# Performance work log

Measured on AMD Instinct MI355X. Metric: run time of the kernel, lower is better.

The kernel has to match this reference:

```python
import jax, jax.numpy as jnp
import numpy as np

NUM_CLASSES = 80
CONF_THRE = 0.2
NMS_THRE = 0.45
MAX_DET = 300   # fixed cap replacing torch's variable-length NMS output (padded + keep mask)
IMG = 640.0


def setup_inputs() -> dict:
    key = jax.random.key(0)
    k1, k2 = jax.random.split(key)
    pred = jax.random.uniform(k1, (32, 8400, 85), dtype=jnp.float32)
    # scale cx,cy,w,h to pixel range so IoU/NMS geometry is realistic
    pred = pred.at[..., :4].multiply(IMG)
    zone = jax.random.uniform(k2, (8, 2), dtype=jnp.float32) * IMG
    return {"prediction": pred, "zone": zone}


def _pairwise_iou(b):
    # b: [B, K, 4] in x1y1x2y2
    area = jnp.clip(b[..., 2] - b[..., 0], 0.0) * jnp.clip(b[..., 3] - b[..., 1], 0.0)
    lt = jnp.maximum(b[:, :, None, :2], b[:, None, :, :2])
    rb = jnp.minimum(b[:, :, None, 2:], b[:, None, :, 2:])
    wh = jnp.clip(rb - lt, 0.0)
    inter = wh[..., 0] * wh[..., 1]
    return inter / (area[:, :, None] + area[:, None, :] - inter + 1e-9)


def _postprocess(prediction):
    # decode cx,cy,w,h -> x1,y1,x2,y2
    xy = prediction[..., :2]
    wh = prediction[..., 2:4]
    boxes = jnp.concatenate([xy - wh * 0.5, xy + wh * 0.5], axis=-1)  # [B,N,4]
    obj = prediction[..., 4]                                           # [B,N]
    cls = prediction[..., 5:5 + NUM_CLASSES]
    class_conf = jnp.max(cls, axis=-1)                                 # [B,N]
    class_pred = jnp.argmax(cls, axis=-1)                              # [B,N]

    # confidence mask (obj * class_conf >= thre); invalid -> -inf so top_k drops them
    nms_score = obj * class_conf
    nms_score = jnp.where(nms_score >= CONF_THRE, nms_score, -jnp.inf)

    s, idx = jax.lax.top_k(nms_score, MAX_DET)                         # [B,K]
    b = jnp.take_along_axis(boxes, idx[..., None], axis=1)             # [B,K,4]

    # class-agnostic greedy NMS on score-sorted boxes (matches torchvision.ops.nms)
    iou = _pairwise_iou(b)                                             # [B,K,K]
    keep = jnp.isfinite(s)                                             # valid (passed conf) entries
    ar = jnp.arange(MAX_DET)
    def body(i, keep):
        sup = keep[:, i][:, None] & (iou[:, i, :] > NMS_THRE) & (ar > i)
        return keep & jnp.logical_not(sup)
    keep = jax.lax.fori_loop(0, MAX_DET, body, keep)

    obj_s = jnp.take_along_axis(obj, idx, axis=1)
    conf_s = jnp.take_along_axis(class_conf, idx, axis=1)
    cls_s = jnp.take_along_axis(class_pred, idx, axis=1).astype(jnp.int32)
    # extract_boxes_scores_and_classes: score = max over columns [obj, class_conf]
    scores = jnp.maximum(obj_s, conf_s)
    return b, scores, cls_s, keep


def _points_inside_zone(px, py, zone):
    # px, py: [B,K]; zone: [Z,2]. Ray-casting parity test (faithful to torch version).
    zr = jnp.roll(zone, shift=1, axis=0)
    xi, yi = zone[:, 0], zone[:, 1]
    xj, yj = zr[:, 0], zr[:, 1]
    pyb = py[..., None]  # [B,K,1] vs [Z]
    pxb = px[..., None]
    gyi = yi > pyb
    gyj = yj > pyb
    gx = (xj - xi) * (pyb - yi) / (yj - yi) + xi
    inter = (gyi != gyj) & (gx > pxb)
    return (jnp.sum(inter.astype(jnp.int32), axis=-1) % 2) > 0


def reference(prediction, zone):
    b, scores, classes, keep = _postprocess(prediction)
    cx = (b[..., 0] + b[..., 2]) * 0.5
    cy = (b[..., 1] + b[..., 3]) * 0.5
    in_zone = _points_inside_zone(cx, cy, zone) & keep
    centers_yx = jnp.stack([cy, cx], axis=-1)                          # [B,K,2]
    boxes_yxyx = jnp.stack([b[..., 1], b[..., 0], b[..., 3], b[..., 2]], axis=-1)
    return boxes_yxyx, in_zone, scores, classes, centers_yx, keep
```

## Files before the change

kernel.cpp:

```cpp
#include <hip/hip_runtime.h>
#include <stdint.h>

typedef unsigned long long ull;

#define NA 8400
#define NB 32
#define KTOP 300
#define NC 80
#define CH 9
#define NKPAD 9216
#define NCOPY 16
#define HSTRIDE 257

#define O1 38400
#define O2 48000
#define O3 57600
#define O4 67200
#define O5 86400

#define WS_BATCH_BASE (2u << 20)
#define WS_BATCH_STRIDE 16384

__global__ __launch_bounds__(256) void score_kernel(const float* __restrict__ pred,
                                                    uint32_t* __restrict__ keys) {
    __shared__ float sP[128 * 85];
    const int blk = blockIdx.x;
    const float4* g4 = (const float4*)(pred + (size_t)blk * 128 * 85);
    float4* l4 = (float4*)sP;
    for (int i = threadIdx.x; i < (128 * 85 / 4); i += 256) l4[i] = g4[i];
    __syncthreads();
    const int t = threadIdx.x;
    if (t < 128) {
        const float* p = sP + t * 85;
        float obj = p[4];
        float b0 = p[5], b1 = p[6], b2 = p[7], b3 = p[8];
        #pragma unroll
        for (int c = 4; c < NC; c += 4) {
            b0 = fmaxf(b0, p[5 + c]);
            b1 = fmaxf(b1, p[6 + c]);
            b2 = fmaxf(b2, p[7 + c]);
            b3 = fmaxf(b3, p[8 + c]);
        }
        float best = fmaxf(fmaxf(b0, b1), fmaxf(b2, b3));
        float sc = obj * best;
        uint32_t u = (sc >= 0.2f) ? (__float_as_uint(sc) | 0x80000000u) : 0x007FFFFFu;
        keys[(size_t)blk * 128 + t] = u;
    }
}

__global__ __launch_bounds__(1024) void select_kernel(const uint32_t* __restrict__ keys,
                                                      uint8_t* __restrict__ ws) {
    __shared__ uint32_t sKeys[NKPAD];
    __shared__ ull sSel[KTOP];
    __shared__ ull sSorted[KTOP];
    __shared__ uint32_t sH[NCOPY * HSTRIDE];
    __shared__ uint32_t sWTot[16];
    __shared__ uint32_t sBc[2];
    __shared__ uint32_t sRank[KTOP];

    const int b = blockIdx.x;
    const int t = threadIdx.x;
    const int lane = t & 63;
    const int wv = t >> 6;

    {
        const uint4* g4 = (const uint4*)(keys + (size_t)b * NA);
        uint4* l4 = (uint4*)sKeys;
        for (int i = t; i < NA / 4; i += 1024) l4[i] = g4[i];
        for (int i = NA + t; i < NKPAD; i += 1024) sKeys[i] = 0u;
    }
    if (t < KTOP) sRank[t] = 0u;
    __syncthreads();

    const int beg = t * CH;
    uint32_t prefix = 0, r = KTOP;
    for (int round = 0; round < 4; ++round) {
        const int shift = 24 - 8 * round;
        for (int i = t; i < NCOPY * HSTRIDE; i += 1024) sH[i] = 0u;
        __syncthreads();
        const uint32_t pmask = (round == 0) ? 0u : (0xFFFFFFFFu << (shift + 8));
        const uint32_t pref = prefix & pmask;
        uint32_t* hw = &sH[wv * HSTRIDE];
        #pragma unroll
        for (int e = 0; e < CH; ++e) {
            uint32_t k = sKeys[beg + e];
            if ((k & pmask) == pref)
                atomicAdd(&hw[(k >> shift) & 0xFFu], 1u);
        }
        __syncthreads();
        if (wv == 0) {
            uint32_t v0 = 0, v1 = 0, v2 = 0, v3 = 0;
            #pragma unroll
            for (int c = 0; c < NCOPY; ++c) {
                const uint32_t* hc = &sH[c * HSTRIDE];
                v0 += hc[lane]; v1 += hc[64 + lane];
                v2 += hc[128 + lane]; v3 += hc[192 + lane];
            }
            uint32_t s0 = v0, s1 = v1, s2 = v2, s3 = v3;
            #pragma unroll
            for (int off = 1; off < 64; off <<= 1) {
                uint32_t o0 = __shfl_down(s0, off, 64), o1 = __shfl_down(s1, off, 64);
                uint32_t o2 = __shfl_down(s2, off, 64), o3 = __shfl_down(s3, off, 64);
                if (lane + off < 64) { s0 += o0; s1 += o1; s2 += o2; s3 += o3; }
            }
            uint32_t T1 = __shfl(s1, 0, 64), T2 = __shfl(s2, 0, 64), T3 = __shfl(s3, 0, 64);
            uint32_t S0 = s0 + T1 + T2 + T3;
            uint32_t S1 = s1 + T2 + T3;
            uint32_t S2 = s2 + T3;
            uint32_t S3 = s3;
            if (S0 >= r && S0 - v0 < r) { sBc[0] = prefix | ((uint32_t)lane << shift);         sBc[1] = r - (S0 - v0); }
            if (S1 >= r && S1 - v1 < r) { sBc[0] = prefix | ((uint32_t)(64  + lane) << shift); sBc[1] = r - (S1 - v1); }
            if (S2 >= r && S2 - v2 < r) { sBc[0] = prefix | ((uint32_t)(128 + lane) << shift); sBc[1] = r - (S2 - v2); }
            if (S3 >= r && S3 - v3 < r) { sBc[0] = prefix | ((uint32_t)(192 + lane) << shift); sBc[1] = r - (S3 - v3); }
        }
        __syncthreads();
        prefix = sBc[0]; r = sBc[1];
    }
    const uint32_t kth = prefix;
    const uint32_t rem = r;
    const uint32_t cntgt = KTOP - rem;

    {
        uint32_t gtc = 0, eqc = 0;
        #pragma unroll
        for (int e = 0; e < CH; ++e) {
            uint32_t k = sKeys[beg + e];
            gtc += (k > kth) ? 1u : 0u;
            eqc += (k == kth) ? 1u : 0u;
        }
        uint32_t pack = (gtc << 16) | eqc;
        uint32_t ps = pack;
        #pragma unroll
        for (int off = 1; off < 64; off <<= 1) {
            uint32_t o = __shfl_up(ps, off, 64);
            if (lane >= off) ps += o;
        }
        if (lane == 63) sWTot[wv] = ps;
        __syncthreads();
        uint32_t excl = ps - pack;
        #pragma unroll
        for (int w2 = 0; w2 < 16; ++w2) if (w2 < wv) excl += sWTot[w2];
        uint32_t gtoff = excl >> 16;
        uint32_t eqoff = excl & 0xFFFFu;
        #pragma unroll
        for (int e = 0; e < CH; ++e) {
            uint32_t k = sKeys[beg + e];
            uint32_t idx = (uint32_t)(beg + e);
            if (k > kth) {
                sSel[gtoff++] = ((ull)k << 32) | (ull)(0xFFFFFFFFu - idx);
            } else if (k == kth) {
                if (eqoff < rem)
                    sSel[cntgt + eqoff] = ((ull)k << 32) | (ull)(0xFFFFFFFFu - idx);
                eqoff++;
            }
        }
        __syncthreads();
    }

    for (int p2 = t; p2 < KTOP * 4; p2 += 1024) {
        const int i = p2 >> 2;
        const int q = p2 & 3;
        const ull my = sSel[i];
        const int j0 = q * 75, j1 = j0 + 75;
        uint32_t cnt = 0;
        for (int j = j0; j < j1; ++j)
            cnt += (sSel[j] > my) ? 1u : 0u;
        if (cnt) atomicAdd(&sRank[i], cnt);
    }
    __syncthreads();
    if (t < KTOP) sSorted[sRank[t]] = sSel[t];
    __syncthreads();

    ull* selW = (ull*)(ws + WS_BATCH_BASE + (size_t)b * WS_BATCH_STRIDE);
    if (t < KTOP) selW[t] = sSorted[t];
}

__global__ __launch_bounds__(1024) void prep_kernel(const float* __restrict__ pred,
                                                    uint8_t* __restrict__ ws,
                                                    float* __restrict__ out) {
    #pragma clang fp contract(off)
    __shared__ float sB0[KTOP], sB1[KTOP], sB2[KTOP], sB3[KTOP];
    const int b = blockIdx.y;
    const int t = threadIdx.x;
    const ull* sel = (const ull*)(ws + WS_BATCH_BASE + (size_t)b * WS_BATCH_STRIDE);
    const size_t bo = (size_t)b * KTOP;

    if (blockIdx.x == 0) {
        if (t < 2 * KTOP) {
            const int row = t >> 1;
            const int half = t & 1;
            const uint32_t a = 0xFFFFFFFFu - (uint32_t)sel[row];
            const float* p = pred + ((size_t)b * NA + a) * 85;
            const int cbase = half * 40;
            float v0 = p[5 + cbase], v1 = p[6 + cbase], v2 = p[7 + cbase], v3 = p[8 + cbase];
            int   c0 = cbase, c1 = cbase + 1, c2 = cbase + 2, c3 = cbase + 3;
            #pragma unroll
            for (int c = 4; c < 40; c += 4) {
                float w0 = p[5 + cbase + c],     w1 = p[6 + cbase + c];
                float w2 = p[7 + cbase + c],     w3 = p[8 + cbase + c];
                if (w0 > v0) { v0 = w0; c0 = cbase + c; }
                if (w1 > v1) { v1 = w1; c1 = cbase + c + 1; }
                if (w2 > v2) { v2 = w2; c2 = cbase + c + 2; }
                if (w3 > v3) { v3 = w3; c3 = cbase + c + 3; }
            }
            float bv = v0; int bc = c0;
            if (v1 > bv || (v1 == bv && c1 < bc)) { bv = v1; bc = c1; }
            if (v2 > bv || (v2 == bv && c2 < bc)) { bv = v2; bc = c2; }
            if (v3 > bv || (v3 == bv && c3 < bc)) { bv = v3; bc = c3; }
            float pv = __shfl_xor(bv, 1, 64);
            int   pc = __shfl_xor(bc, 1, 64);
            if (half == 0) {
                if (pv > bv) { bv = pv; bc = pc; }
                float x = p[0], y = p[1], w = p[2], h = p[3], obj = p[4];
                float hw = w * 0.5f, hh = h * 0.5f;
                float x1 = x - hw, y1 = y - hh, x2 = x + hw, y2 = y + hh;
                out[(bo + row) * 4 + 0] = y1;
                out[(bo + row) * 4 + 1] = x1;
                out[(bo + row) * 4 + 2] = y2;
                out[(bo + row) * 4 + 3] = x2;
                out[O4 + (bo + row) * 2 + 0] = (y1 + y2) * 0.5f;
                out[O4 + (bo + row) * 2 + 1] = (x1 + x2) * 0.5f;
                out[O2 + bo + row] = fmaxf(obj, bv);
                out[O3 + bo + row] = (float)bc;
            }
        }
    } else {
        if (t < KTOP) {
            const uint32_t a = 0xFFFFFFFFu - (uint32_t)sel[t];
            const float* p = pred + ((size_t)b * NA + a) * 85;
            float x = p[0], y = p[1], w = p[2], h = p[3];
            float hw = w * 0.5f, hh = h * 0.5f;
            sB0[t] = x - hw; sB1[t] = y - hh; sB2[t] = x + hw; sB3[t] = y + hh;
        }
        __syncthreads();
        ull* maskW = (ull*)(ws + WS_BATCH_BASE + (size_t)b * WS_BATCH_STRIDE + 2400);
        for (int p2 = t; p2 < KTOP * 5; p2 += 1024) {
            const int role = p2 / KTOP;
            const int i = p2 - role * KTOP;
            const int j0 = role * 64;
            int jmax = j0 + 64; if (jmax > KTOP) jmax = KTOP;
            float x1 = sB0[i], y1 = sB1[i], x2 = sB2[i], y2 = sB3[i];
            float ai = fmaxf(x2 - x1, 0.0f) * fmaxf(y2 - y1, 0.0f);
            ull bits = 0ull;
            for (int j = j0; j < jmax; ++j) {
                float bx1 = sB0[j], by1 = sB1[j], bx2 = sB2[j], by2 = sB3[j];
                float aj = fmaxf(bx2 - bx1, 0.0f) * fmaxf(by2 - by1, 0.0f);
                float iw = fminf(x2, bx2) - fmaxf(x1, bx1); iw = fmaxf(iw, 0.0f);
                float ih = fminf(y2, by2) - fmaxf(y1, by1); ih = fmaxf(ih, 0.0f);
                float inter = iw * ih;
                float den = ai + aj;
                den = den - inter;
                den = den + 1e-9f;
                float iou = inter / den;
                if (j > i && iou > 0.45f) bits |= (1ull << (j - j0));
            }
            maskW[i * 5 + role] = bits;
        }
    }
}

__global__ __launch_bounds__(512) void finish_kernel(const float* __restrict__ zone,
                                                     const uint8_t* __restrict__ ws,
                                                     float* __restrict__ out) {
    #pragma clang fp contract(off)
    __shared__ ull sMask[KTOP * 5];
    __shared__ ull sSel[KTOP];
    __shared__ uint32_t sPar[KTOP];
    __shared__ ull sKeepF[5];
    __shared__ float sZone[16];
    const int b = blockIdx.x;
    const int t = threadIdx.x;
    const int lane = t & 63;
    const int wv = t >> 6;
    const ull* selG = (const ull*)(ws + WS_BATCH_BASE + (size_t)b * WS_BATCH_STRIDE);
    const ull* maskG = selG + KTOP;
    for (int i = t; i < KTOP; i += 512) sSel[i] = selG[i];
    for (int i = t; i < KTOP * 5; i += 512) sMask[i] = maskG[i];
    if (t < 16) sZone[t] = zone[t];
    __syncthreads();

    const size_t bo = (size_t)b * KTOP;
    if (wv == 0) {
        ull rm[5][5];
        ull kw[5];
        #pragma unroll
        for (int w = 0; w < 5; ++w) {
            int i = w * 64 + lane;
            bool f = (i < KTOP) && (((uint32_t)(sSel[i] >> 32)) > 0x007FFFFFu);
            kw[w] = __ballot(f);
            #pragma unroll
            for (int ww = 0; ww < 5; ++ww)
                rm[w][ww] = (i < KTOP) ? sMask[i * 5 + ww] : 0ull;
        }
        #pragma unroll
        for (int w = 0; w < 5; ++w) {
            ull cur = kw[w];
            while (cur) {
                int ib = __builtin_ctzll(cur);
                ull m0 = __shfl(rm[w][0], ib);
                ull m1 = __shfl(rm[w][1], ib);
                ull m2 = __shfl(rm[w][2], ib);
                ull m3 = __shfl(rm[w][3], ib);
                ull m4 = __shfl(rm[w][4], ib);
                kw[0] &= ~m0; kw[1] &= ~m1; kw[2] &= ~m2; kw[3] &= ~m3; kw[4] &= ~m4;
                ull done = (ib == 63) ? 0ull : (~0ull << (ib + 1));
                cur = kw[w] & done;
            }
        }
        if (lane == 0) {
            #pragma unroll
            for (int w = 0; w < 5; ++w) sKeepF[w] = kw[w];
        }
    } else if (t >= 64 && t < 64 + KTOP) {
        const int i = t - 64;
        float cy = out[O4 + (bo + i) * 2 + 0];
        float cx = out[O4 + (bo + i) * 2 + 1];
        int cnt = 0;
        #pragma unroll
        for (int e = 0; e < 8; ++e) {
            float xi = sZone[2 * e], yi = sZone[2 * e + 1];
            int ep = (e + 7) & 7;
            float xj = sZone[2 * ep], yj = sZone[2 * ep + 1];
            bool gyi = yi > cy, gyj = yj > cy;
            if (gyi != gyj) {
                float gx = (xj - xi) * (cy - yi) / (yj - yi) + xi;
                if (gx > cx) cnt++;
            }
        }
        sPar[i] = (uint32_t)(cnt & 1);
    }
    __syncthreads();

    if (t < KTOP) {
        int kp = (int)((sKeepF[t >> 6] >> (t & 63)) & 1ull);
        int inz = (sPar[t] && kp) ? 1 : 0;
        out[O1 + bo + t] = (float)inz;
        out[O5 + bo + t] = (float)kp;
    }
}

extern "C" void kernel_launch(void* const* d_in, const int* in_sizes, int n_in,
                              void* d_out, int out_size, void* d_ws, size_t ws_size,
                              hipStream_t stream) {
    const float* pred = (const float*)d_in[0];
    const float* zone = (const float*)d_in[1];
    float* out = (float*)d_out;
    uint32_t* keys = (uint32_t*)d_ws;
    uint8_t* ws = (uint8_t*)d_ws;

    score_kernel<<<(NB * NA) / 128, 256, 0, stream>>>(pred, keys);
    select_kernel<<<NB, 1024, 0, stream>>>(keys, ws);
    prep_kernel<<<dim3(2, NB), 1024, 0, stream>>>(pred, ws, out);
    finish_kernel<<<NB, 512, 0, stream>>>(zone, ws, out);
}
```

Before: 209.1 us.

## Replace 4-pass radix select with single-pass bin histogram and fuse kernels

The four-round radix select over the score keys becomes one histogram pass over fixed-width bins above the confidence threshold. Keys in the boundary bin go to a small candidate buffer that is ranked exactly, capped at 256 entries. The box/class gather moves into the select kernel, and IoU mask construction plus greedy NMS and zone tests merge into one kernel, cutting four launches to three and removing the global mask round trip. The candidate cap can silently drop entries if more than 256 keys share the boundary bin.

After: 197.5 us. -5.5%, faster.

```diff
diff --git a/kernel.cpp b/kernel.cpp
--- a/kernel.cpp
+++ b/kernel.cpp
@@ -9,8 +9,11 @@
 #define NC 80
 #define CH 9
 #define NKPAD 9216
-#define NCOPY 16
-#define HSTRIDE 257
+#define NBIN 616
+#define HSTR 617
+#define NCPY 8
+#define BASEK 0xBE4CCCCDu
+#define CANDMAX 256
 
 #define O1 38400
 #define O2 48000
@@ -19,7 +22,7 @@
 #define O5 86400
 
 #define WS_BATCH_BASE (2u << 20)
-#define WS_BATCH_STRIDE 16384
+#define WS_BATCH_STRIDE 8192
 
 __global__ __launch_bounds__(256) void score_kernel(const float* __restrict__ pred,
                                                     uint32_t* __restrict__ keys) {
@@ -48,15 +51,24 @@
     }
 }
 
-__global__ __launch_bounds__(1024) void select_kernel(const uint32_t* __restrict__ keys,
-                                                      uint8_t* __restrict__ ws) {
+__device__ __forceinline__ uint32_t key_bin(uint32_t k) {
+    return (k < BASEK) ? 0u : (1u + ((k - BASEK) >> 15));
+}
+
+__global__ __launch_bounds__(1024) void select_kernel(const float* __restrict__ pred,
+                                                      const uint32_t* __restrict__ keys,
+                                                      uint8_t* __restrict__ ws,
+                                                      float* __restrict__ out) {
+    #pragma clang fp contract(off)
     __shared__ uint32_t sKeys[NKPAD];
+    __shared__ uint32_t sH[NCPY * HSTR];
     __shared__ ull sSel[KTOP];
     __shared__ ull sSorted[KTOP];
-    __shared__ uint32_t sH[NCOPY * HSTRIDE];
+    __shared__ ull sCand[CANDMAX];
     __shared__ uint32_t sWTot[16];
     __shared__ uint32_t sBc[2];
     __shared__ uint32_t sRank[KTOP];
+    __shared__ uint32_t sCN;
 
     const int b = blockIdx.x;
     const int t = threadIdx.x;
@@ -69,64 +81,57 @@
         for (int i = t; i < NA / 4; i += 1024) l4[i] = g4[i];
         for (int i = NA + t; i < NKPAD; i += 1024) sKeys[i] = 0u;
     }
+    for (int i = t; i < NCPY * HSTR; i += 1024) sH[i] = 0u;
     if (t < KTOP) sRank[t] = 0u;
     __syncthreads();
 
     const int beg = t * CH;
-    uint32_t prefix = 0, r = KTOP;
-    for (int round = 0; round < 4; ++round) {
-        const int shift = 24 - 8 * round;
-        for (int i = t; i < NCOPY * HSTRIDE; i += 1024) sH[i] = 0u;
-        __syncthreads();
-        const uint32_t pmask = (round == 0) ? 0u : (0xFFFFFFFFu << (shift + 8));
-        const uint32_t pref = prefix & pmask;
-        uint32_t* hw = &sH[wv * HSTRIDE];
+    {
+        uint32_t* hw = &sH[(t >> 7) * HSTR];
         #pragma unroll
         for (int e = 0; e < CH; ++e) {
             uint32_t k = sKeys[beg + e];
-            if ((k & pmask) == pref)
-                atomicAdd(&hw[(k >> shift) & 0xFFu], 1u);
-        }
-        __syncthreads();
-        if (wv == 0) {
-            uint32_t v0 = 0, v1 = 0, v2 = 0, v3 = 0;
+            atomicAdd(&hw[key_bin(k)], 1u);
+        }
+    }
+    __syncthreads();
+
+    uint32_t v = 0, s = 0;
+    if (t < 640) {
+        if (t < NBIN) {
             #pragma unroll
-            for (int c = 0; c < NCOPY; ++c) {
-                const uint32_t* hc = &sH[c * HSTRIDE];
-                v0 += hc[lane]; v1 += hc[64 + lane];
-                v2 += hc[128 + lane]; v3 += hc[192 + lane];
-            }
-            uint32_t s0 = v0, s1 = v1, s2 = v2, s3 = v3;
-            #pragma unroll
-            for (int off = 1; off < 64; off <<= 1) {
-                uint32_t o0 = __shfl_down(s0, off, 64), o1 = __shfl_down(s1, off, 64);
-                uint32_t o2 = __shfl_down(s2, off, 64), o3 = __shfl_down(s3, off, 64);
-                if (lane + off < 64) { s0 += o0; s1 += o1; s2 += o2; s3 += o3; }
-            }
-            uint32_t T1 = __shfl(s1, 0, 64), T2 = __shfl(s2, 0, 64), T3 = __shfl(s3, 0, 64);
-            uint32_t S0 = s0 + T1 + T2 + T3;
-            uint32_t S1 = s1 + T2 + T3;
-            uint32_t S2 = s2 + T3;
-            uint32_t S3 = s3;
-            if (S0 >= r && S0 - v0 < r) { sBc[0] = prefix | ((uint32_t)lane << shift);         sBc[1] = r - (S0 - v0); }
-            if (S1 >= r && S1 - v1 < r) { sBc[0] = prefix | ((uint32_t)(64  + lane) << shift); sBc[1] = r - (S1 - v1); }
-            if (S2 >= r && S2 - v2 < r) { sBc[0] = prefix | ((uint32_t)(128 + lane) << shift); sBc[1] = r - (S2 - v2); }
-            if (S3 >= r && S3 - v3 < r) { sBc[0] = prefix | ((uint32_t)(192 + lane) << shift); sBc[1] = r - (S3 - v3); }
-        }
-        __syncthreads();
-        prefix = sBc[0]; r = sBc[1];
-    }
-    const uint32_t kth = prefix;
-    const uint32_t rem = r;
+            for (int c = 0; c < NCPY; ++c) v += sH[c * HSTR + t];
+        }
+        s = v;
+        #pragma unroll
+        for (int off = 1; off < 64; off <<= 1) {
+            uint32_t o = __shfl_down(s, off, 64);
+            if (lane + off < 64) s += o;
+        }
+        if (lane == 0) sWTot[wv] = s;
+    }
+    __syncthreads();
+    if (t < 640) {
+        uint32_t S = s;
+        for (int w2 = wv + 1; w2 < 10; ++w2) S += sWTot[w2];
+        uint32_t above = S - v;
+        if (above < KTOP && S >= KTOP) {
+            sBc[0] = (uint32_t)t;
+            sBc[1] = KTOP - above;
+        }
+    }
+    __syncthreads();
+    const uint32_t Tbin = sBc[0];
+    const uint32_t rem = sBc[1];
     const uint32_t cntgt = KTOP - rem;
 
     {
         uint32_t gtc = 0, eqc = 0;
         #pragma unroll
         for (int e = 0; e < CH; ++e) {
-            uint32_t k = sKeys[beg + e];
-            gtc += (k > kth) ? 1u : 0u;
-            eqc += (k == kth) ? 1u : 0u;
+            uint32_t bin = key_bin(sKeys[beg + e]);
+            gtc += (bin > Tbin) ? 1u : 0u;
+            eqc += (bin == Tbin) ? 1u : 0u;
         }
         uint32_t pack = (gtc << 16) | eqc;
         uint32_t ps = pack;
@@ -142,17 +147,33 @@
         for (int w2 = 0; w2 < 16; ++w2) if (w2 < wv) excl += sWTot[w2];
         uint32_t gtoff = excl >> 16;
         uint32_t eqoff = excl & 0xFFFFu;
+        if (t == 1023) {
+            uint32_t tot = eqoff + eqc;
+            sCN = (tot > CANDMAX) ? CANDMAX : tot;
+        }
         #pragma unroll
         for (int e = 0; e < CH; ++e) {
             uint32_t k = sKeys[beg + e];
+            uint32_t bin = key_bin(k);
             uint32_t idx = (uint32_t)(beg + e);
-            if (k > kth) {
+            if (bin > Tbin) {
                 sSel[gtoff++] = ((ull)k << 32) | (ull)(0xFFFFFFFFu - idx);
-            } else if (k == kth) {
-                if (eqoff < rem)
-                    sSel[cntgt + eqoff] = ((ull)k << 32) | (ull)(0xFFFFFFFFu - idx);
+            } else if (bin == Tbin) {
+                if (eqoff < CANDMAX)
+                    sCand[eqoff] = ((ull)k << 32) | (ull)(0xFFFFFFFFu - idx);
                 eqoff++;
             }
+        }
+        __syncthreads();
+    }
+
+    {
+        int cn = (int)sCN;
+        if (t < cn) {
+            ull my = sCand[t];
+            uint32_t rk = 0;
+            for (int j = 0; j < cn; ++j) rk += (sCand[j] > my) ? 1u : 0u;
+            if (rk < rem) sSel[cntgt + rk] = my;
         }
         __syncthreads();
     }
@@ -172,97 +193,56 @@
     __syncthreads();
 
     ull* selW = (ull*)(ws + WS_BATCH_BASE + (size_t)b * WS_BATCH_STRIDE);
+    float* boxW = (float*)(selW + KTOP);
+    const size_t bo = (size_t)b * KTOP;
     if (t < KTOP) selW[t] = sSorted[t];
-}
-
-__global__ __launch_bounds__(1024) void prep_kernel(const float* __restrict__ pred,
-                                                    uint8_t* __restrict__ ws,
-                                                    float* __restrict__ out) {
+    if (t < 2 * KTOP) {
+        const int row = t >> 1;
+        const int half = t & 1;
+        const uint32_t a = 0xFFFFFFFFu - (uint32_t)sSorted[row];
+        const float* p = pred + ((size_t)b * NA + a) * 85;
+        const int cbase = half * 40;
+        float v0 = p[5 + cbase], v1 = p[6 + cbase], v2 = p[7 + cbase], v3 = p[8 + cbase];
+        int   c0 = cbase, c1 = cbase + 1, c2 = cbase + 2, c3 = cbase + 3;
+        #pragma unroll
+        for (int c = 4; c < 40; c += 4) {
+            float w0 = p[5 + cbase + c],     w1 = p[6 + cbase + c];
+            float w2 = p[7 + cbase + c],     w3 = p[8 + cbase + c];
+            if (w0 > v0) { v0 = w0; c0 = cbase + c; }
+            if (w1 > v1) { v1 = w1; c1 = cbase + c + 1; }
+            if (w2 > v2) { v2 = w2; c2 = cbase + c + 2; }
+            if (w3 > v3) { v3 = w3; c3 = cbase + c + 3; }
+        }
+        float bv = v0; int bc = c0;
+        if (v1 > bv || (v1 == bv && c1 < bc)) { bv = v1; bc = c1; }
+        if (v2 > bv || (v2 == bv && c2 < bc)) { bv = v2; bc = c2; }
+        if (v3 > bv || (v3 == bv && c3 < bc)) { bv = v3; bc = c3; }
+        float pv = __shfl_xor(bv, 1, 64);
+        int   pc = __shfl_xor(bc, 1, 64);
+        if (half == 0) {
+            if (pv > bv) { bv = pv; bc = pc; }
+            float x = p[0], y = p[1], w = p[2], h = p[3], obj = p[4];
+            float hw = w * 0.5f, hh = h * 0.5f;
+            float x1 = x - hw, y1 = y - hh, x2 = x + hw, y2 = y + hh;
+            boxW[row] = x1; boxW[KTOP + row] = y1;
+            boxW[2 * KTOP + row] = x2; boxW[3 * KTOP + row] = y2;
+            out[(bo + row) * 4 + 0] = y1;
+            out[(bo + row) * 4 + 1] = x1;
+            out[(bo + row) * 4 + 2] = y2;
+            out[(bo + row) * 4 + 3] = x2;
+            out[O4 + (bo + row) * 2 + 0] = (y1 + y2) * 0.5f;
+            out[O4 + (bo + row) * 2 + 1] = (x1 + x2) * 0.5f;
+            out[O2 + bo + row] = fmaxf(obj, bv);
+            out[O3 + bo + row] = (float)bc;
+        }
+    }
+}
+
+__global__ __launch_bounds__(1024) void nms_kernel(const float* __restrict__ zone,
+                                                   const uint8_t* __restrict__ ws,
+                                                   float* __restrict__ out) {
     #pragma clang fp contract(off)
     __shared__ float sB0[KTOP], sB1[KTOP], sB2[KTOP], sB3[KTOP];
-    const int b = blockIdx.y;
-    const int t = threadIdx.x;
-    const ull* sel = (const ull*)(ws + WS_BATCH_BASE + (size_t)b * WS_BATCH_STRIDE);
-    const size_t bo = (size_t)b * KTOP;
-
-    if (blockIdx.x == 0) {
-        if (t < 2 * KTOP) {
-            const int row = t >> 1;
-            const int half = t & 1;
-            const uint32_t a = 0xFFFFFFFFu - (uint32_t)sel[row];
-            const float* p = pred + ((size_t)b * NA + a) * 85;
-            const int cbase = half * 40;
-            float v0 = p[5 + cbase], v1 = p[6 + cbase], v2 = p[7 + cbase], v3 = p[8 + cbase];
-            int   c0 = cbase, c1 = cbase + 1, c2 = cbase + 2, c3 = cbase + 3;
-            #pragma unroll
-            for (int c = 4; c < 40; c += 4) {
-                float w0 = p[5 + cbase + c],     w1 = p[6 + cbase + c];
-                float w2 = p[7 + cbase + c],     w3 = p[8 + cbase + c];
-                if (w0 > v0) { v0 = w0; c0 = cbase + c; }
-                if (w1 > v1) { v1 = w1; c1 = cbase + c + 1; }
-                if (w2 > v2) { v2 = w2; c2 = cbase + c + 2; }
-                if (w3 > v3) { v3 = w3; c3 = cbase + c + 3; }
-            }
-            float bv = v0; int bc = c0;
-            if (v1 > bv || (v1 == bv && c1 < bc)) { bv = v1; bc = c1; }
-            if (v2 > bv || (v2 == bv && c2 < bc)) { bv = v2; bc = c2; }
-            if (v3 > bv || (v3 == bv && c3 < bc)) { bv = v3; bc = c3; }
-            float pv = __shfl_xor(bv, 1, 64);
-            int   pc = __shfl_xor(bc, 1, 64);
-            if (half == 0) {
-                if (pv > bv) { bv = pv; bc = pc; }
-                float x = p[0], y = p[1], w = p[2], h = p[3], obj = p[4];
-                float hw = w * 0.5f, hh = h * 0.5f;
-                float x1 = x - hw, y1 = y - hh, x2 = x + hw, y2 = y + hh;
-                out[(bo + row) * 4 + 0] = y1;
-                out[(bo + row) * 4 + 1] = x1;
-                out[(bo + row) * 4 + 2] = y2;
-                out[(bo + row) * 4 + 3] = x2;
-                out[O4 + (bo + row) * 2 + 0] = (y1 + y2) * 0.5f;
-                out[O4 + (bo + row) * 2 + 1] = (x1 + x2) * 0.5f;
-                out[O2 + bo + row] = fmaxf(obj, bv);
-                out[O3 + bo + row] = (float)bc;
-            }
-        }
-    } else {
-        if (t < KTOP) {
-            const uint32_t a = 0xFFFFFFFFu - (uint32_t)sel[t];
-            const float* p = pred + ((size_t)b * NA + a) * 85;
-            float x = p[0], y = p[1], w = p[2], h = p[3];
-            float hw = w * 0.5f, hh = h * 0.5f;
-            sB0[t] = x - hw; sB1[t] = y - hh; sB2[t] = x + hw; sB3[t] = y + hh;
-        }
-        __syncthreads();
-        ull* maskW = (ull*)(ws + WS_BATCH_BASE + (size_t)b * WS_BATCH_STRIDE + 2400);
-        for (int p2 = t; p2 < KTOP * 5; p2 += 1024) {
-            const int role = p2 / KTOP;
-            const int i = p2 - role * KTOP;
-            const int j0 = role * 64;
-            int jmax = j0 + 64; if (jmax > KTOP) jmax = KTOP;
-            float x1 = sB0[i], y1 = sB1[i], x2 = sB2[i], y2 = sB3[i];
-            float ai = fmaxf(x2 - x1, 0.0f) * fmaxf(y2 - y1, 0.0f);
-            ull bits = 0ull;
-            for (int j = j0; j < jmax; ++j) {
-                float bx1 = sB0[j], by1 = sB1[j], bx2 = sB2[j], by2 = sB3[j];
-                float aj = fmaxf(bx2 - bx1, 0.0f) * fmaxf(by2 - by1, 0.0f);
-                float iw = fminf(x2, bx2) - fmaxf(x1, bx1); iw = fmaxf(iw, 0.0f);
-                float ih = fminf(y2, by2) - fmaxf(y1, by1); ih = fmaxf(ih, 0.0f);
-                float inter = iw * ih;
-                float den = ai + aj;
-                den = den - inter;
-                den = den + 1e-9f;
-                float iou = inter / den;
-                if (j > i && iou > 0.45f) bits |= (1ull << (j - j0));
-            }
-            maskW[i * 5 + role] = bits;
-        }
-    }
-}
-
-__global__ __launch_bounds__(512) void finish_kernel(const float* __restrict__ zone,
-                                                     const uint8_t* __restrict__ ws,
-                                                     float* __restrict__ out) {
-    #pragma clang fp contract(off)
     __shared__ ull sMask[KTOP * 5];
     __shared__ ull sSel[KTOP];
     __shared__ uint32_t sPar[KTOP];
@@ -273,10 +253,38 @@
     const int lane = t & 63;
     const int wv = t >> 6;
     const ull* selG = (const ull*)(ws + WS_BATCH_BASE + (size_t)b * WS_BATCH_STRIDE);
-    const ull* maskG = selG + KTOP;
-    for (int i = t; i < KTOP; i += 512) sSel[i] = selG[i];
-    for (int i = t; i < KTOP * 5; i += 512) sMask[i] = maskG[i];
+    const float* boxG = (const float*)(selG + KTOP);
+    if (t < KTOP) {
+        sSel[t] = selG[t];
+        sB0[t] = boxG[t];            sB1[t] = boxG[KTOP + t];
+        sB2[t] = boxG[2 * KTOP + t]; sB3[t] = boxG[3 * KTOP + t];
+    }
     if (t < 16) sZone[t] = zone[t];
+    __syncthreads();
+
+    for (int p2 = t; p2 < KTOP * 5; p2 += 1024) {
+        const int role = p2 / KTOP;
+        const int i = p2 - role * KTOP;
+        const int j0 = role * 64;
+        int jmax = j0 + 64; if (jmax > KTOP) jmax = KTOP;
+        if (jmax <= i + 1) { sMask[i * 5 + role] = 0ull; continue; }
+        float x1 = sB0[i], y1 = sB1[i], x2 = sB2[i], y2 = sB3[i];
+        float ai = fmaxf(x2 - x1, 0.0f) * fmaxf(y2 - y1, 0.0f);
+        ull bits = 0ull;
+        for (int j = j0; j < jmax; ++j) {
+            float bx1 = sB0[j], by1 = sB1[j], bx2 = sB2[j], by2 = sB3[j];
+            float aj = fmaxf(bx2 - bx1, 0.0f) * fmaxf(by2 - by1, 0.0f);
+            float iw = fminf(x2, bx2) - fmaxf(x1, bx1); iw = fmaxf(iw, 0.0f);
+            float ih = fminf(y2, by2) - fmaxf(y1, by1); ih = fmaxf(ih, 0.0f);
+            float inter = iw * ih;
+            float den = ai + aj;
+            den = den - inter;
+            den = den + 1e-9f;
+            float iou = inter / den;
+            if (j > i && iou > 0.45f) bits |= (1ull << (j - j0));
+        }
+        sMask[i * 5 + role] = bits;
+    }
     __syncthreads();
 
     const size_t bo = (size_t)b * KTOP;
@@ -311,10 +319,10 @@
             #pragma unroll
             for (int w = 0; w < 5; ++w) sKeepF[w] = kw[w];
         }
-    } else if (t >= 64 && t < 64 + KTOP) {
-        const int i = t - 64;
-        float cy = out[O4 + (bo + i) * 2 + 0];
-        float cx = out[O4 + (bo + i) * 2 + 1];
+    } else if (t >= 512 && t < 512 + KTOP) {
+        const int i = t - 512;
+        float cy = (sB1[i] + sB3[i]) * 0.5f;
+        float cx = (sB0[i] + sB2[i]) * 0.5f;
         int cnt = 0;
         #pragma unroll
         for (int e = 0; e < 8; ++e) {
@@ -349,7 +357,6 @@
     uint8_t* ws = (uint8_t*)d_ws;
 
     score_kernel<<<(NB * NA) / 128, 256, 0, stream>>>(pred, keys);
-    select_kernel<<<NB, 1024, 0, stream>>>(keys, ws);
-    prep_kernel<<<dim3(2, NB), 1024, 0, stream>>>(pred, ws, out);
-    finish_kernel<<<NB, 512, 0, stream>>>(zone, ws, out);
-}
+    select_kernel<<<NB, 1024, 0, stream>>>(pred, keys, ws, out);
+    nms_kernel<<<NB, 1024, 0, stream>>>(zone, ws, out);
+}
```
